# Kernel optimization log

Measured on AMD Instinct MI355X. Metric: run time of the kernel, lower is better.

The kernel has to match this reference:

```python
import jax, jax.numpy as jnp
import numpy as np

N_NODES = 50000
N_GRAPHS = 64
HIDDEN = 128
INPUT = 128
NEG_SLOPE = 0.2


def _gat_layer(x, src, dst, W, a_src, a_dst, b, n_nodes):
    # x: [N, Fin]; src/dst: [E] (self-loops already included)
    h = x @ W                              # [N, H]
    alpha_s = h @ a_src                    # [N]
    alpha_d = h @ a_dst                    # [N]
    e = alpha_s[src] + alpha_d[dst]        # [E]
    e = jnp.where(e > 0, e, NEG_SLOPE * e)  # leaky_relu(0.2)
    # segment softmax over destination node
    m = jax.ops.segment_max(e, dst, num_segments=n_nodes)  # [N]
    m = jnp.where(jnp.isfinite(m), m, 0.0)
    ee = jnp.exp(e - m[dst])
    s = jax.ops.segment_sum(ee, dst, num_segments=n_nodes)
    coef = ee / (s[dst] + 1e-16)           # [E]
    out = jax.ops.segment_sum(h[src] * coef[:, None], dst, num_segments=n_nodes)
    return out + b


def setup_inputs() -> dict:
    key = jax.random.key(0)
    ks = jax.random.split(key, 16)
    x = jax.random.normal(ks[0], (N_NODES, INPUT), dtype=jnp.float32)
    edge_index = jax.random.randint(ks[1], (2, 600000), 0, N_NODES, dtype=jnp.int64 if jax.config.x64_enabled else jnp.int32).astype(jnp.int32)
    batch = jnp.sort(jax.random.randint(ks[2], (N_NODES,), 0, N_GRAPHS)).astype(jnp.int32)
    def glorot(k, shape):
        lim = float(np.sqrt(6.0 / (shape[0] + shape[-1])))
        return jax.random.uniform(k, shape, jnp.float32, -lim, lim)
    params = {}
    dims = [(INPUT, HIDDEN), (HIDDEN, HIDDEN), (HIDDEN, HIDDEN)]
    for i, (fi, fo) in enumerate(dims, 1):
        params[f"W{i}"] = glorot(ks[3 * i], (fi, fo))
        params[f"a_src{i}"] = glorot(ks[3 * i + 1], (fo,)) * 0.1
        params[f"a_dst{i}"] = glorot(ks[3 * i + 2], (fo,)) * 0.1
        params[f"b{i}"] = jnp.zeros((fo,), jnp.float32)
    return dict(x=x, edge_index=edge_index, batch=batch, **params)


def reference(x, edge_index, batch,
              W1, a_src1, a_dst1, b1,
              W2, a_src2, a_dst2, b2,
              W3, a_src3, a_dst3, b3):
    n = x.shape[0]
    loops = jnp.arange(n, dtype=edge_index.dtype)
    src = jnp.concatenate([edge_index[0], loops])  # PyG add_self_loops=True
    dst = jnp.concatenate([edge_index[1], loops])
    h = jax.nn.elu(_gat_layer(x, src, dst, W1, a_src1, a_dst1, b1, n))
    h = jax.nn.elu(_gat_layer(h, src, dst, W2, a_src2, a_dst2, b2, n))
    h = jax.nn.elu(_gat_layer(h, src, dst, W3, a_src3, a_dst3, b3, n))
    # global_mean_pool
    sums = jax.ops.segment_sum(h, batch, num_segments=N_GRAPHS)
    cnt = jax.ops.segment_sum(jnp.ones((n,), h.dtype), batch, num_segments=N_GRAPHS)
    return sums / jnp.maximum(cnt, 1.0)[:, None]
```

## Files before the change

### kernel.cpp

```cpp
#include <hip/hip_runtime.h>
#include <math.h>

#define N_NODES 50000
#define N_GRAPHS 64
#define HID 128
#define SCAN_B 196
#define NODE_BLKS 196
#define NBUCK 128
#define AP 132

typedef _Float16 half8 __attribute__((ext_vector_type(8)));
typedef float f32x4 __attribute__((ext_vector_type(4)));
typedef int i32x4 __attribute__((ext_vector_type(4)));

__device__ __forceinline__ float lrelu(float e) { return e > 0.f ? e : 0.2f * e; }
__device__ __forceinline__ float elu_fast(float o) { return o > 0.f ? o : __expf(o) - 1.f; }

__device__ __forceinline__ void fmix_lo(float& a, int h2, float c) {
    asm("v_fma_mix_f32 %0, %1, %2, %0 op_sel_hi:[1,0,0]" : "+v"(a) : "v"(h2), "v"(c));
}
__device__ __forceinline__ void fmix_hi(float& a, int h2, float c) {
    asm("v_fma_mix_f32 %0, %1, %2, %0 op_sel:[1,0,0] op_sel_hi:[1,0,0]" : "+v"(a) : "v"(h2), "v"(c));
}

__global__ void count_prep(const int* __restrict__ dst, int n_e, int nblk,
                           int* __restrict__ counts, int* __restrict__ epos,
                           int* __restrict__ start,
                           int* __restrict__ dhist, int* __restrict__ gcur,
                           const float* __restrict__ W0, const float* __restrict__ W1,
                           const float* __restrict__ W2,
                           const float* __restrict__ as0, const float* __restrict__ ad0,
                           const float* __restrict__ as1, const float* __restrict__ ad1,
                           const float* __restrict__ as2, const float* __restrict__ ad2,
                           _Float16* __restrict__ Wh0, _Float16* __restrict__ Wh1,
                           _Float16* __restrict__ Wh2,
                           float* __restrict__ wfold) {
    int blk = blockIdx.x;
    if (blk < nblk) {
        if (blk == 0) {
            if (threadIdx.x <= N_GRAPHS) start[threadIdx.x] = -1;
            if (threadIdx.x < NBUCK) { dhist[threadIdx.x] = 0; gcur[threadIdx.x] = 0; }
        }
        int e = blk * 256 + threadIdx.x;
        if (e < n_e) epos[e] = atomicAdd(&counts[dst[e]], 1);
        return;
    }
    int b = blk - nblk;
    if (b < 24) {
        int layer = b >> 3;
        const float* W = layer == 0 ? W0 : (layer == 1 ? W1 : W2);
        _Float16* Wh = layer == 0 ? Wh0 : (layer == 1 ? Wh1 : Wh2);
        int t = (b & 7) * 256 + threadIdx.x;
        int lane = t & 63;
        int nt = (t >> 6) & 7;
        int kt = t >> 9;
        int n = nt * 16 + (lane & 15);
        int kbase = kt * 32 + (lane >> 4) * 8;
#pragma unroll
        for (int j = 0; j < 8; ++j) {
            float w = W[(size_t)(kbase + j) * 128 + n];
            Wh[(size_t)t * 8 + j] = (_Float16)w;
        }
    } else {
        int idx = b - 24;
        int layer = idx >> 1, which = idx & 1;
        const float* W = layer == 0 ? W0 : (layer == 1 ? W1 : W2);
        const float* a = which == 0 ? (layer == 0 ? as0 : (layer == 1 ? as1 : as2))
                                    : (layer == 0 ? ad0 : (layer == 1 ? ad1 : ad2));
        int k = threadIdx.x;
        if (k < 128) {
            float s = 0.f;
            for (int j = 0; j < 128; ++j) s = fmaf(W[k * 128 + j], a[j], s);
            wfold[idx * 128 + k] = s;
        }
    }
}

__global__ __launch_bounds__(256) void block_reduce(const int* __restrict__ counts,
                                                    int* __restrict__ bsum) {
    __shared__ int red[256];
    int t = threadIdx.x;
    int i = blockIdx.x * 256 + t;
    red[t] = (i < N_NODES) ? counts[i] : 0;
    __syncthreads();
#pragma unroll
    for (int off = 128; off; off >>= 1) {
        if (t < off) red[t] += red[t + off];
        __syncthreads();
    }
    if (t == 0) bsum[blockIdx.x] = red[0];
}

__global__ __launch_bounds__(256) void block_scan(const int* __restrict__ counts,
                                                  const int* __restrict__ bsum,
                                                  const int* __restrict__ batch,
                                                  int* __restrict__ offs,
                                                  int* __restrict__ start,
                                                  int* __restrict__ dhist) {
    __shared__ int sb[256];
    __shared__ int sh[256];
    __shared__ int lh[NBUCK];
    int t = threadIdx.x;
    if (t < NBUCK) lh[t] = 0;
    int v = (t < SCAN_B) ? bsum[t] : 0;
    sb[t] = v;
    __syncthreads();
#pragma unroll
    for (int off = 1; off < 256; off <<= 1) {
        int u = (t >= off) ? sb[t - off] : 0;
        __syncthreads();
        sb[t] += u;
        __syncthreads();
    }
    int bpre = (blockIdx.x == 0) ? 0 : sb[blockIdx.x - 1];
    if (blockIdx.x == 0 && t == SCAN_B - 1) offs[N_NODES] = sb[t];

    int i = blockIdx.x * 256 + t;
    int c = (i < N_NODES) ? counts[i] : 0;
    sh[t] = c;
    __syncthreads();
#pragma unroll
    for (int off = 1; off < 256; off <<= 1) {
        int u = (t >= off) ? sh[t - off] : 0;
        __syncthreads();
        sh[t] += u;
        __syncthreads();
    }
    if (i < N_NODES) {
        int e = bpre + sh[t] - c;
        offs[i] = e;
        int b = batch[i];
        if (i == 0) start[b] = 0;
        else if (batch[i - 1] != b) start[b] = i;
        atomicAdd(&lh[c < NBUCK - 1 ? c : NBUCK - 1], 1);
    }
    __syncthreads();
    if (t < NBUCK) {
        int n = lh[t];
        if (n) atomicAdd(&dhist[t], n);
    }
}

__global__ __launch_bounds__(256) void scatter_kernel(const int* __restrict__ src,
                                                      const int* __restrict__ dst, int n_e,
                                                      const int* __restrict__ epos,
                                                      int* __restrict__ csr_src,
                                                      float* __restrict__ outz,
                                                      const int* __restrict__ offs,
                                                      const int* __restrict__ dhist,
                                                      int* __restrict__ gcur,
                                                      int* __restrict__ order) {
    int gid = blockIdx.x * 256 + threadIdx.x;
    if (gid < N_GRAPHS * HID) outz[gid] = 0.f;
    if (gid < n_e) {
        int d = dst[gid];
        csr_src[offs[d] + epos[gid]] = src[gid];
    }
    if (blockIdx.x >= NODE_BLKS) return;

    __shared__ int lh[NBUCK], sc[NBUCK], lbase[NBUCK];
    int t = threadIdx.x;
    if (t < NBUCK) lh[t] = 0;
    __syncthreads();
    int b = -1, lpos = 0;
    if (gid < N_NODES) {
        int deg = offs[gid + 1] - offs[gid];
        b = deg < NBUCK - 1 ? deg : NBUCK - 1;
        lpos = atomicAdd(&lh[b], 1);
    }
    __syncthreads();
    if (t < NBUCK) sc[t] = dhist[t];
    __syncthreads();
    for (int off = 1; off < NBUCK; off <<= 1) {
        int u = (t < NBUCK && t >= off) ? sc[t - off] : 0;
        __syncthreads();
        if (t < NBUCK) sc[t] += u;
        __syncthreads();
    }
    if (t < NBUCK) {
        int excl = t ? sc[t - 1] : 0;
        int cnt = lh[t];
        int bb = cnt ? atomicAdd(&gcur[t], cnt) : 0;
        lbase[t] = excl + bb;
    }
    __syncthreads();
    if (gid < N_NODES) order[lbase[b] + lpos] = gid;
}

__global__ __launch_bounds__(256) void gemm_mfma(const float* __restrict__ X,
                                                 const _Float16* __restrict__ Wh,
                                                 const float* __restrict__ wsv,
                                                 const float* __restrict__ wdv,
                                                 _Float16* __restrict__ H16,
                                                 float* __restrict__ AS,
                                                 float* __restrict__ AD) {
    __shared__ float wsL[128], wdL[128];
    int t = threadIdx.x;
    if (t < 128) wsL[t] = wsv[t];
    else if (t < 256) wdL[t - 128] = wdv[t - 128];
    __syncthreads();

    int wave = t >> 6, lane = t & 63;
    int m15 = lane & 15, quad = lane >> 4;
    int rowbase = blockIdx.x * 64 + wave * 16;
    int arow = rowbase + m15;
    bool arow_ok = arow < N_NODES;

    f32x4 acc[8];
#pragma unroll
    for (int nt = 0; nt < 8; ++nt) acc[nt] = (f32x4){0.f, 0.f, 0.f, 0.f};
    float as_p = 0.f, ad_p = 0.f;

    const float* xrow = X + (size_t)arow * 128 + quad * 8;
#pragma unroll
    for (int kt = 0; kt < 4; ++kt) {
        f32x4 a0 = (f32x4){0.f, 0.f, 0.f, 0.f};
        f32x4 a1 = (f32x4){0.f, 0.f, 0.f, 0.f};
        if (arow_ok) {
            a0 = *(const f32x4*)(xrow + kt * 32);
            a1 = *(const f32x4*)(xrow + kt * 32 + 4);
        }
        int kb = kt * 32 + quad * 8;
        half8 ah;
#pragma unroll
        for (int j = 0; j < 4; ++j) {
            as_p = fmaf(a0[j], wsL[kb + j], as_p);
            ad_p = fmaf(a0[j], wdL[kb + j], ad_p);
            as_p = fmaf(a1[j], wsL[kb + 4 + j], as_p);
            ad_p = fmaf(a1[j], wdL[kb + 4 + j], ad_p);
            ah[j] = (_Float16)a0[j];
            ah[4 + j] = (_Float16)a1[j];
        }
#pragma unroll
        for (int nt = 0; nt < 8; ++nt) {
            size_t fidx = ((size_t)((kt * 8 + nt) * 64 + lane)) * 8;
            half8 bh = *(const half8*)(Wh + fidx);
            acc[nt] = __builtin_amdgcn_mfma_f32_16x16x32_f16(ah, bh, acc[nt], 0, 0, 0);
        }
    }

#pragma unroll
    for (int nt = 0; nt < 8; ++nt) {
        int c = nt * 16 + m15;
#pragma unroll
        for (int reg = 0; reg < 4; ++reg) {
            int gr = rowbase + quad * 4 + reg;
            if (gr < N_NODES) H16[(size_t)gr * 128 + c] = (_Float16)acc[nt][reg];
        }
    }
    as_p += __shfl_xor(as_p, 16);
    ad_p += __shfl_xor(ad_p, 16);
    as_p += __shfl_xor(as_p, 32);
    ad_p += __shfl_xor(ad_p, 32);
    if (quad == 0 && arow_ok) { AS[arow] = as_p; AD[arow] = ad_p; }
}

__global__ __launch_bounds__(256) void aggregate_kernel(const _Float16* __restrict__ H16,
                                                        const float* __restrict__ AS,
                                                        const float* __restrict__ AD,
                                                        const int* __restrict__ offs,
                                                        const int* __restrict__ csr_src,
                                                        const int* __restrict__ order,
                                                        const float* __restrict__ bias,
                                                        const _Float16* __restrict__ Whn,
                                                        const float* __restrict__ wfn,
                                                        _Float16* __restrict__ Hn,
                                                        float* __restrict__ ASn,
                                                        float* __restrict__ ADn,
                                                        float* __restrict__ OUT) {
    __shared__ int2 sh_sp[16][64];
    __shared__ _Float16 aW[16][AP];
    __shared__ int nds[16];
    int tid = threadIdx.x;
    int quad = tid >> 4;
    int l16 = tid & 15;
    int node = order[blockIdx.x * 16 + quad];

    int beg = offs[node];
    int deg = offs[node + 1] - beg;
    float ad = AD[node];
    float eself = lrelu(AS[node] + ad);
    const i32x4* H4 = (const i32x4*)H16;
    i32x4 hsv = H4[(size_t)node * 16 + l16];
    bool fast = deg <= 64;

    float m, ssum = 0.f, ps;
    if (fast) {
        float mym = -INFINITY;
        for (int i = l16; i < deg; i += 16) {
            int sv = csr_src[beg + i];
            float e = lrelu(AS[sv] + ad);
            sh_sp[quad][i] = make_int2(sv, __float_as_int(e));
            mym = fmaxf(mym, e);
        }
#pragma unroll
        for (int off = 8; off; off >>= 1) mym = fmaxf(mym, __shfl_xor(mym, off, 16));
        m = fmaxf(mym, eself);
        ps = __expf(eself - m);
        for (int i = l16; i < deg; i += 16) {
            int2 sp = sh_sp[quad][i];
            float p = __expf(__int_as_float(sp.y) - m);
            sh_sp[quad][i] = make_int2(sp.x, __float_as_int(p));
            ssum += p;
        }
    } else {
        float mym = -INFINITY;
        for (int i = beg + l16; i < beg + deg; i += 16)
            mym = fmaxf(mym, lrelu(AS[csr_src[i]] + ad));
#pragma unroll
        for (int off = 8; off; off >>= 1) mym = fmaxf(mym, __shfl_xor(mym, off, 16));
        m = fmaxf(mym, eself);
        ps = __expf(eself - m);
        for (int i = beg + l16; i < beg + deg; i += 16)
            ssum += __expf(lrelu(AS[csr_src[i]] + ad) - m);
    }

    float accA[8] = {0.f, 0.f, 0.f, 0.f, 0.f, 0.f, 0.f, 0.f};
    float accB[8] = {0.f, 0.f, 0.f, 0.f, 0.f, 0.f, 0.f, 0.f};

    if (fast) {
        int k = 0;
        for (; k + 3 < deg; k += 4) {
            int2 sp0 = sh_sp[quad][k];
            int2 sp1 = sh_sp[quad][k + 1];
            int2 sp2 = sh_sp[quad][k + 2];
            int2 sp3 = sh_sp[quad][k + 3];
            i32x4 h0 = H4[(size_t)sp0.x * 16 + l16];
            i32x4 h1 = H4[(size_t)sp1.x * 16 + l16];
            i32x4 h2 = H4[(size_t)sp2.x * 16 + l16];
            i32x4 h3 = H4[(size_t)sp3.x * 16 + l16];
            float c0 = __int_as_float(sp0.y), c1 = __int_as_float(sp1.y);
            float c2 = __int_as_float(sp2.y), c3 = __int_as_float(sp3.y);
#pragma unroll
            for (int j = 0; j < 4; ++j) {
                fmix_lo(accA[2 * j], h0[j], c0);
                fmix_hi(accA[2 * j + 1], h0[j], c0);
                fmix_lo(accB[2 * j], h1[j], c1);
                fmix_hi(accB[2 * j + 1], h1[j], c1);
            }
#pragma unroll
            for (int j = 0; j < 4; ++j) {
                fmix_lo(accA[2 * j], h2[j], c2);
                fmix_hi(accA[2 * j + 1], h2[j], c2);
                fmix_lo(accB[2 * j], h3[j], c3);
                fmix_hi(accB[2 * j + 1], h3[j], c3);
            }
        }
        for (; k < deg; ++k) {
            int2 sp0 = sh_sp[quad][k];
            float c0 = __int_as_float(sp0.y);
            i32x4 h0 = H4[(size_t)sp0.x * 16 + l16];
#pragma unroll
            for (int j = 0; j < 4; ++j) {
                fmix_lo(accA[2 * j], h0[j], c0);
                fmix_hi(accA[2 * j + 1], h0[j], c0);
            }
        }
    } else {
        for (int k = 0; k < deg; ++k) {
            int s = csr_src[beg + k];
            float c = __expf(lrelu(AS[s] + ad) - m);
            i32x4 h0 = H4[(size_t)s * 16 + l16];
#pragma unroll
            for (int j = 0; j < 4; ++j) {
                fmix_lo(accA[2 * j], h0[j], c);
                fmix_hi(accA[2 * j + 1], h0[j], c);
            }
        }
    }

#pragma unroll
    for (int j = 0; j < 4; ++j) {
        fmix_lo(accA[2 * j], hsv[j], ps);
        fmix_hi(accA[2 * j + 1], hsv[j], ps);
    }
#pragma unroll
    for (int off = 8; off; off >>= 1) ssum += __shfl_xor(ssum, off, 16);
    float inv = __builtin_amdgcn_rcpf(ssum + ps + 1e-16f);

    int c0i = l16 * 8;
    f32x4 b0 = ((const f32x4*)bias)[l16 * 2];
    f32x4 b1 = ((const f32x4*)bias)[l16 * 2 + 1];
    f32x4 o0, o1;
    o0.x = elu_fast(fmaf(accA[0] + accB[0], inv, b0.x));
    o0.y = elu_fast(fmaf(accA[1] + accB[1], inv, b0.y));
    o0.z = elu_fast(fmaf(accA[2] + accB[2], inv, b0.z));
    o0.w = elu_fast(fmaf(accA[3] + accB[3], inv, b0.w));
    o1.x = elu_fast(fmaf(accA[4] + accB[4], inv, b1.x));
    o1.y = elu_fast(fmaf(accA[5] + accB[5], inv, b1.y));
    o1.z = elu_fast(fmaf(accA[6] + accB[6], inv, b1.z));
    o1.w = elu_fast(fmaf(accA[7] + accB[7], inv, b1.w));
    if (OUT) {
        ((f32x4*)OUT)[(size_t)node * 32 + l16 * 2] = o0;
        ((f32x4*)OUT)[(size_t)node * 32 + l16 * 2 + 1] = o1;
    }

    if (Whn) {
        const float* wsn = wfn;
        const float* wdn = wfn + 128;
        float asn = o0.x * wsn[c0i] + o0.y * wsn[c0i + 1] + o0.z * wsn[c0i + 2] +
                    o0.w * wsn[c0i + 3] + o1.x * wsn[c0i + 4] + o1.y * wsn[c0i + 5] +
                    o1.z * wsn[c0i + 6] + o1.w * wsn[c0i + 7];
        float adn = o0.x * wdn[c0i] + o0.y * wdn[c0i + 1] + o0.z * wdn[c0i + 2] +
                    o0.w * wdn[c0i + 3] + o1.x * wdn[c0i + 4] + o1.y * wdn[c0i + 5] +
                    o1.z * wdn[c0i + 6] + o1.w * wdn[c0i + 7];
#pragma unroll
        for (int off = 8; off; off >>= 1) {
            asn += __shfl_xor(asn, off, 16);
            adn += __shfl_xor(adn, off, 16);
        }
        if (l16 == 0) {
            ASn[node] = asn;
            ADn[node] = adn;
            nds[quad] = node;
        }
        half8 hh;
        hh[0] = (_Float16)o0.x; hh[1] = (_Float16)o0.y;
        hh[2] = (_Float16)o0.z; hh[3] = (_Float16)o0.w;
        hh[4] = (_Float16)o1.x; hh[5] = (_Float16)o1.y;
        hh[6] = (_Float16)o1.z; hh[7] = (_Float16)o1.w;
        *(half8*)&aW[quad][c0i] = hh;
        __syncthreads();

        int wv = tid >> 6, lane = tid & 63;
        int m15 = lane & 15, eq = lane >> 4;
        f32x4 acc0 = (f32x4){0.f, 0.f, 0.f, 0.f};
        f32x4 acc1 = (f32x4){0.f, 0.f, 0.f, 0.f};
#pragma unroll
        for (int kt = 0; kt < 4; ++kt) {
            half8 ah = *(const half8*)&aW[m15][kt * 32 + eq * 8];
            half8 bh0 = *(const half8*)(Whn + ((size_t)((kt * 8 + wv * 2) * 64 + lane)) * 8);
            half8 bh1 = *(const half8*)(Whn + ((size_t)((kt * 8 + wv * 2 + 1) * 64 + lane)) * 8);
            acc0 = __builtin_amdgcn_mfma_f32_16x16x32_f16(ah, bh0, acc0, 0, 0, 0);
            acc1 = __builtin_amdgcn_mfma_f32_16x16x32_f16(ah, bh1, acc1, 0, 0, 0);
        }
#pragma unroll
        for (int reg = 0; reg < 4; ++reg) {
            int nid = nds[eq * 4 + reg];
            Hn[(size_t)nid * 128 + wv * 32 + m15] = (_Float16)acc0[reg];
            Hn[(size_t)nid * 128 + wv * 32 + 16 + m15] = (_Float16)acc1[reg];
        }
    }
}

__device__ __forceinline__ int estart(const int* __restrict__ start, int g) {
    for (; g < N_GRAPHS; ++g) {
        int v = start[g];
        if (v >= 0) return v;
    }
    return N_NODES;
}

__global__ __launch_bounds__(128) void pool_kernel(const float* __restrict__ F,
                                                   const int* __restrict__ start,
                                                   float* __restrict__ out) {
    int b = blockIdx.x;
    int g = b >> 4, sub = b & 15;
    int c = threadIdx.x;
    int s0 = estart(start, g), e0 = estart(start, g + 1);
    float acc = 0.f;
    for (int i = s0 + sub; i < e0; i += 16) acc += F[(size_t)i * 128 + c];
    int cnt = e0 - s0;
    float r = 1.f / (float)(cnt > 1 ? cnt : 1);
    atomicAdd(&out[(size_t)g * 128 + c], acc * r);
}

extern "C" void kernel_launch(void* const* d_in, const int* in_sizes, int n_in,
                              void* d_out, int out_size, void* d_ws, size_t ws_size,
                              hipStream_t stream) {
    const float* x = (const float*)d_in[0];
    const int* edge_index = (const int*)d_in[1];
    const int* batch = (const int*)d_in[2];
    const float* W[3]   = {(const float*)d_in[3], (const float*)d_in[7], (const float*)d_in[11]};
    const float* avs[3] = {(const float*)d_in[4], (const float*)d_in[8], (const float*)d_in[12]};
    const float* avd[3] = {(const float*)d_in[5], (const float*)d_in[9], (const float*)d_in[13]};
    const float* bb[3]  = {(const float*)d_in[6], (const float*)d_in[10], (const float*)d_in[14]};
    int E0 = in_sizes[1] / 2;
    const int* esrc = edge_index;
    const int* edst = edge_index + E0;

    char* p = (char*)d_ws;
    auto alloc = [&](size_t bytes) -> void* {
        void* q = (void*)p;
        p += (bytes + 255) & ~(size_t)255;
        return q;
    };
    int* counts   = (int*)alloc((size_t)N_NODES * 4);
    int* offs     = (int*)alloc((size_t)(N_NODES + 1) * 4);
    int* epos     = (int*)alloc((size_t)E0 * 4);
    int* csr_src  = (int*)alloc((size_t)E0 * 4);
    int* start    = (int*)alloc((N_GRAPHS + 1) * 4);
    int* bsum     = (int*)alloc(SCAN_B * 4);
    int* dhist    = (int*)alloc(NBUCK * 4);
    int* gcur     = (int*)alloc(NBUCK * 4);
    int* order    = (int*)alloc((size_t)N_NODES * 4);
    float* ASa    = (float*)alloc((size_t)N_NODES * 4);
    float* ADa    = (float*)alloc((size_t)N_NODES * 4);
    float* ASb    = (float*)alloc((size_t)N_NODES * 4);
    float* ADb    = (float*)alloc((size_t)N_NODES * 4);
    float* wfold  = (float*)alloc(6 * 128 * 4);
    _Float16* Ha  = (_Float16*)alloc((size_t)N_NODES * HID * 2);
    _Float16* Hb  = (_Float16*)alloc((size_t)N_NODES * HID * 2);
    float* FA     = (float*)alloc((size_t)N_NODES * HID * 4);
    _Float16* Wh[3];
    for (int l = 0; l < 3; ++l) Wh[l] = (_Float16*)alloc(16384 * 2);

    int nblk = (E0 + 255) / 256;
    hipMemsetAsync(counts, 0, (size_t)N_NODES * 4, stream);
    count_prep<<<nblk + 30, 256, 0, stream>>>(edst, E0, nblk, counts, epos, start, dhist, gcur,
                                              W[0], W[1], W[2], avs[0], avd[0], avs[1], avd[1],
                                              avs[2], avd[2], Wh[0], Wh[1], Wh[2], wfold);
    block_reduce<<<SCAN_B, 256, 0, stream>>>(counts, bsum);
    block_scan<<<SCAN_B, 256, 0, stream>>>(counts, bsum, batch, offs, start, dhist);
    scatter_kernel<<<nblk, 256, 0, stream>>>(esrc, edst, E0, epos, csr_src, (float*)d_out,
                                             offs, dhist, gcur, order);

    gemm_mfma<<<(N_NODES + 63) / 64, 256, 0, stream>>>(x, Wh[0], wfold, wfold + 128,
                                                       Ha, ASa, ADa);
    aggregate_kernel<<<N_NODES / 16, 256, 0, stream>>>(Ha, ASa, ADa, offs, csr_src, order,
                                                       bb[0], Wh[1], wfold + 2 * 128,
                                                       Hb, ASb, ADb, nullptr);
    aggregate_kernel<<<N_NODES / 16, 256, 0, stream>>>(Hb, ASb, ADb, offs, csr_src, order,
                                                       bb[1], Wh[2], wfold + 4 * 128,
                                                       Ha, ASa, ADa, nullptr);
    aggregate_kernel<<<N_NODES / 16, 256, 0, stream>>>(Ha, ASa, ADa, offs, csr_src, order,
                                                       bb[2], nullptr, nullptr,
                                                       nullptr, nullptr, nullptr, FA);

    pool_kernel<<<N_GRAPHS * 16, 128, 0, stream>>>(FA, start, (float*)d_out);
}
```

Before: 258.6 us.

## Shard per-destination edge counters across eight copies to reduce atomic contention

The edge-count histogram is split into eight shards chosen by block index, so atomics from different blocks land on different counters. The scan kernels then sum the shards and write a per-node, per-shard base offset that the scatter kernel adds when placing each edge in CSR order. The aim is less contention on the global atomic increments. In exchange the memset grows eightfold and the reduce, scan and scatter kernels do extra reads and writes.

```diff
diff --git a/kernel.cpp b/kernel.cpp
--- a/kernel.cpp
+++ b/kernel.cpp
@@ -8,6 +8,7 @@
 #define NODE_BLKS 196
 #define NBUCK 128
 #define AP 132
+#define NSHARD 8
 
 typedef _Float16 half8 __attribute__((ext_vector_type(8)));
 typedef float f32x4 __attribute__((ext_vector_type(4)));
@@ -24,7 +25,7 @@
 }
 
 __global__ void count_prep(const int* __restrict__ dst, int n_e, int nblk,
-                           int* __restrict__ counts, int* __restrict__ epos,
+                           int* __restrict__ counts8, int* __restrict__ epos,
                            int* __restrict__ start,
                            int* __restrict__ dhist, int* __restrict__ gcur,
                            const float* __restrict__ W0, const float* __restrict__ W1,
@@ -41,8 +42,9 @@
             if (threadIdx.x <= N_GRAPHS) start[threadIdx.x] = -1;
             if (threadIdx.x < NBUCK) { dhist[threadIdx.x] = 0; gcur[threadIdx.x] = 0; }
         }
+        int shard = blk & (NSHARD - 1);
         int e = blk * 256 + threadIdx.x;
-        if (e < n_e) epos[e] = atomicAdd(&counts[dst[e]], 1);
+        if (e < n_e) epos[e] = atomicAdd(&counts8[shard * N_NODES + dst[e]], 1);
         return;
     }
     int b = blk - nblk;
@@ -76,12 +78,17 @@
     }
 }
 
-__global__ __launch_bounds__(256) void block_reduce(const int* __restrict__ counts,
+__global__ __launch_bounds__(256) void block_reduce(const int* __restrict__ counts8,
                                                     int* __restrict__ bsum) {
     __shared__ int red[256];
     int t = threadIdx.x;
     int i = blockIdx.x * 256 + t;
-    red[t] = (i < N_NODES) ? counts[i] : 0;
+    int c = 0;
+    if (i < N_NODES) {
+#pragma unroll
+        for (int s = 0; s < NSHARD; ++s) c += counts8[s * N_NODES + i];
+    }
+    red[t] = c;
     __syncthreads();
 #pragma unroll
     for (int off = 128; off; off >>= 1) {
@@ -91,10 +98,11 @@
     if (t == 0) bsum[blockIdx.x] = red[0];
 }
 
-__global__ __launch_bounds__(256) void block_scan(const int* __restrict__ counts,
+__global__ __launch_bounds__(256) void block_scan(const int* __restrict__ counts8,
                                                   const int* __restrict__ bsum,
                                                   const int* __restrict__ batch,
                                                   int* __restrict__ offs,
+                                                  int* __restrict__ sbase,
                                                   int* __restrict__ start,
                                                   int* __restrict__ dhist) {
     __shared__ int sb[256];
@@ -116,7 +124,20 @@
     if (blockIdx.x == 0 && t == SCAN_B - 1) offs[N_NODES] = sb[t];
 
     int i = blockIdx.x * 256 + t;
-    int c = (i < N_NODES) ? counts[i] : 0;
+    int c = 0;
+    if (i < N_NODES) {
+        int cs[NSHARD];
+        int run = 0;
+#pragma unroll
+        for (int s = 0; s < NSHARD; ++s) {
+            cs[s] = run;
+            run += counts8[s * N_NODES + i];
+        }
+        c = run;
+        i32x4* sb4 = (i32x4*)(sbase + (size_t)i * NSHARD);
+        sb4[0] = (i32x4){cs[0], cs[1], cs[2], cs[3]};
+        sb4[1] = (i32x4){cs[4], cs[5], cs[6], cs[7]};
+    }
     sh[t] = c;
     __syncthreads();
 #pragma unroll
@@ -144,6 +165,7 @@
 __global__ __launch_bounds__(256) void scatter_kernel(const int* __restrict__ src,
                                                       const int* __restrict__ dst, int n_e,
                                                       const int* __restrict__ epos,
+                                                      const int* __restrict__ sbase,
                                                       int* __restrict__ csr_src,
                                                       float* __restrict__ outz,
                                                       const int* __restrict__ offs,
@@ -154,7 +176,8 @@
     if (gid < N_GRAPHS * HID) outz[gid] = 0.f;
     if (gid < n_e) {
         int d = dst[gid];
-        csr_src[offs[d] + epos[gid]] = src[gid];
+        int shard = (gid >> 8) & (NSHARD - 1);
+        csr_src[offs[d] + sbase[(size_t)d * NSHARD + shard] + epos[gid]] = src[gid];
     }
     if (blockIdx.x >= NODE_BLKS) return;
 
@@ -485,9 +508,10 @@
         p += (bytes + 255) & ~(size_t)255;
         return q;
     };
-    int* counts   = (int*)alloc((size_t)N_NODES * 4);
+    int* counts8  = (int*)alloc((size_t)NSHARD * N_NODES * 4);
     int* offs     = (int*)alloc((size_t)(N_NODES + 1) * 4);
     int* epos     = (int*)alloc((size_t)E0 * 4);
+    int* sbase    = (int*)alloc((size_t)N_NODES * NSHARD * 4);
     int* csr_src  = (int*)alloc((size_t)E0 * 4);
     int* start    = (int*)alloc((N_GRAPHS + 1) * 4);
     int* bsum     = (int*)alloc(SCAN_B * 4);
@@ -506,14 +530,14 @@
     for (int l = 0; l < 3; ++l) Wh[l] = (_Float16*)alloc(16384 * 2);
 
     int nblk = (E0 + 255) / 256;
-    hipMemsetAsync(counts, 0, (size_t)N_NODES * 4, stream);
-    count_prep<<<nblk + 30, 256, 0, stream>>>(edst, E0, nblk, counts, epos, start, dhist, gcur,
+    hipMemsetAsync(counts8, 0, (size_t)NSHARD * N_NODES * 4, stream);
+    count_prep<<<nblk + 30, 256, 0, stream>>>(edst, E0, nblk, counts8, epos, start, dhist, gcur,
                                               W[0], W[1], W[2], avs[0], avd[0], avs[1], avd[1],
                                               avs[2], avd[2], Wh[0], Wh[1], Wh[2], wfold);
-    block_reduce<<<SCAN_B, 256, 0, stream>>>(counts, bsum);
-    block_scan<<<SCAN_B, 256, 0, stream>>>(counts, bsum, batch, offs, start, dhist);
-    scatter_kernel<<<nblk, 256, 0, stream>>>(esrc, edst, E0, epos, csr_src, (float*)d_out,
-                                             offs, dhist, gcur, order);
+    block_reduce<<<SCAN_B, 256, 0, stream>>>(counts8, bsum);
+    block_scan<<<SCAN_B, 256, 0, stream>>>(counts8, bsum, batch, offs, sbase, start, dhist);
+    scatter_kernel<<<nblk, 256, 0, stream>>>(esrc, edst, E0, epos, sbase, csr_src,
+                                             (float*)d_out, offs, dhist, gcur, order);
 
     gemm_mfma<<<(N_NODES + 63) / 64, 256, 0, stream>>>(x, Wh[0], wfold, wfold + 128,
                                                        Ha, ASa, ADa);
```

Measured after the change: 260.1 us. Within noise of the previous version (+0.6%).
